# Performance work log

Hardware: AMD Instinct MI355X
Metric: run time of the kernel (lower is better)

Reference implementation:

```python
import jax, jax.numpy as jnp
import numpy as np

B = 4
MAX_N = 2048
D = 512
H = 8
HD = D // H
SRC_LENS = [2048, 1536, 1800, 1200]   # sum = 6584
REF_LENS = [1900, 2048, 1400, 1600]   # sum = 6948
NEG_INF = -1e9


def setup_inputs() -> dict:
    key = jax.random.key(0)
    ks = jax.random.split(key, 8)
    n_src, n_ref = sum(SRC_LENS), sum(REF_LENS)
    s = 0.02
    return {
        "feats_src": jax.random.normal(ks[0], (n_src, D), dtype=jnp.float32),
        "batch_src": jnp.asarray(np.repeat(np.arange(B), SRC_LENS), dtype=jnp.int32),
        "feats_ref": jax.random.normal(ks[1], (n_ref, D), dtype=jnp.float32),
        "batch_ref": jnp.asarray(np.repeat(np.arange(B), REF_LENS), dtype=jnp.int32),
        "w_in": jax.random.normal(ks[2], (3 * D, D), dtype=jnp.float32) * s,
        "b_in": jnp.zeros((3 * D,), dtype=jnp.float32),
        "w_out": jax.random.normal(ks[3], (D, D), dtype=jnp.float32) * s,
        "b_out": jnp.zeros((D,), dtype=jnp.float32),
        "gw1": jax.random.normal(ks[4], (D, D), dtype=jnp.float32) * s,
        "gb1": jnp.zeros((D,), dtype=jnp.float32),
        "gw2": jax.random.normal(ks[5], (1, D), dtype=jnp.float32) * s,
        "gb2": jnp.zeros((1,), dtype=jnp.float32),
    }


def _to_dense(feats, batch_idx):
    # sparse [N, D] (sorted batch indices) -> dense [B, MAX_N, D] + key_padding_mask
    n = feats.shape[0]
    counts = jax.ops.segment_sum(jnp.ones((n,), jnp.int32), batch_idx, num_segments=B)
    starts = jnp.concatenate([jnp.zeros((1,), jnp.int32), jnp.cumsum(counts)[:-1].astype(jnp.int32)])
    pos = jnp.arange(n, dtype=jnp.int32) - starts[batch_idx]  # position within batch
    dense = jnp.zeros((B, MAX_N, feats.shape[1]), feats.dtype).at[batch_idx, pos].set(feats)
    mask = jnp.arange(MAX_N)[None, :] >= counts[:, None]  # True = padding (key_padding_mask)
    return dense, mask, pos


def reference(feats_src, batch_src, feats_ref, batch_ref,
              w_in, b_in, w_out, b_out, gw1, gb1, gw2, gb2):
    d_src, mask_src, pos_src = _to_dense(feats_src, batch_src)
    d_ref, mask_ref, _ = _to_dense(feats_ref, batch_ref)

    # nn.MultiheadAttention (batch_first, eval mode): packed in_proj, scaled dot-product
    q = (d_src @ w_in[:D].T + b_in[:D]).reshape(B, MAX_N, H, HD)
    k = (d_ref @ w_in[D:2 * D].T + b_in[D:2 * D]).reshape(B, MAX_N, H, HD)
    v = (d_ref @ w_in[2 * D:].T + b_in[2 * D:]).reshape(B, MAX_N, H, HD)
    scores = jnp.einsum('bqhd,bkhd->bhqk', q * (HD ** -0.5), k)
    scores = jnp.where(mask_ref[:, None, None, :], NEG_INF, scores)
    attn = jax.nn.softmax(scores, axis=-1)
    ctx = jnp.einsum('bhqk,bkhd->bqhd', attn, v).reshape(B, MAX_N, D)
    d_aligned = ctx @ w_out.T + b_out

    # gate MLP: Linear -> ReLU -> Linear -> Sigmoid
    gate = jax.nn.sigmoid(jax.nn.relu(d_aligned @ gw1.T + gb1) @ gw2.T + gb2)  # [B, MAX_N, 1]
    d_out = d_src + gate * d_aligned

    # dense -> ragged: gather each token back to its flat slot
    out_flat = d_out[batch_src, pos_src]  # [N_src, D]
    return out_flat, gate
```

## Files before the change

### kernel.cpp

```cpp
#include <hip/hip_runtime.h>
#include <hip/hip_bf16.h>


typedef __bf16 bf16x8_t __attribute__((ext_vector_type(8)));
typedef __bf16 bf16x4_t __attribute__((ext_vector_type(4)));
typedef float f32x4_t __attribute__((ext_vector_type(4)));
typedef float f32x2_t __attribute__((ext_vector_type(2)));

#define CQ_SCALE 0.18033688011112042f

__device__ inline bf16x8_t zero8() {
  bf16x8_t z;
#pragma unroll
  for (int t = 0; t < 8; ++t) z[t] = (__bf16)0.0f;
  return z;
}

__device__ __forceinline__ int sniff_f32(const void* w) {
  unsigned short u = ((const unsigned short*)w)[threadIdx.x & 63];
  return __ballot((u & 0x7F80) >= 0x3F80) != 0ULL;
}

__device__ __forceinline__ int2 swz(int bid, int nwg, int nby) {
  int chunk = nwg >> 3;
  int w = (bid & 7) * chunk + (bid >> 3);
  return make_int2(w / nby, w % nby);
}

__global__ void sentinel_k(float* out) {
  if (threadIdx.x == 0 && blockIdx.x == 0) out[0] = 1000.0f;
}

__global__ void cv_all(const void* w_in, const void* b_in, const void* w_out,
                       const void* b_out, const void* gw1, const void* gb1,
                       const void* gw2, const void* gb2,
                       __hip_bfloat16* __restrict__ ws,
                       const void* fs, const void* fr, int do_feats) {
  int f = sniff_f32(w_in);
  int bid = blockIdx.x;
  if (do_feats && bid < 3383) {
    int i = bid * 256 + threadIdx.x;
    const int NFS = 421376;
    const void* src;
    size_t dst;
    int off;
    if (i < NFS) { src = fs; dst = 11803680; off = i * 8; }
    else { src = fr; dst = 15174688; off = (i - NFS) * 8; }
    __hip_bfloat16* d = ws + dst + off;
    if (f) {
      const float* p = (const float*)src + off;
      bf16x8_t v;
#pragma unroll
      for (int e = 0; e < 8; ++e) v[e] = (__bf16)p[e];
      *reinterpret_cast<bf16x8_t*>(d) = v;
    } else {
      *reinterpret_cast<bf16x8_t*>(d) =
          *reinterpret_cast<const bf16x8_t*>((const __hip_bfloat16*)src + off);
    }
    return;
  }
  int base = do_feats ? 3383 : 0;
  int nb = gridDim.x - base;
  const size_t F_W_IN = 16, F_B_IN = 786448, F_W_OUT = 787984, F_B_OUT = 1050128,
               F_GW1 = 1050640, F_GB1 = 1312784, F_GW2 = 1313296, F_GB2 = 1313808;
  const int total = 1313793;
  for (int g = (bid - base) * 256 + threadIdx.x; g < total; g += nb * 256) {
    const void* src;
    size_t dst;
    int i;
    if (g < 786432) { src = w_in; dst = F_W_IN; i = g; }
    else if (g < 787968) { src = b_in; dst = F_B_IN; i = g - 786432; }
    else if (g < 1050112) { src = w_out; dst = F_W_OUT; i = g - 787968; }
    else if (g < 1050624) { src = b_out; dst = F_B_OUT; i = g - 1050112; }
    else if (g < 1312768) { src = gw1; dst = F_GW1; i = g - 1050624; }
    else if (g < 1313280) { src = gb1; dst = F_GB1; i = g - 1312768; }
    else if (g < 1313792) { src = gw2; dst = F_GW2; i = g - 1313280; }
    else { src = gb2; dst = F_GB2; i = g - 1313792; }
    ws[dst + i] = f ? __float2bfloat16(((const float*)src)[i])
                    : ((const __hip_bfloat16*)src)[i];
  }
}

__device__ __forceinline__ void gemm_core(
    const void* __restrict__ A_, long aoff, const __hip_bfloat16* __restrict__ Bt,
    const __hip_bfloat16* __restrict__ bias, __hip_bfloat16* __restrict__ C,
    int M, int K, int lda, int ldc, float cscale, int relu, int f, int bm, int bn,
    long chs, __bf16 (&As)[128][72], __bf16 (&Bs)[128][72]) {
  int tid = threadIdx.x, lane = tid & 63, wave = tid >> 6;
  int wm = wave >> 1, wn = wave & 1;
  int l15 = lane & 15, quad = lane >> 4;

  f32x4_t acc[4][4];
#pragma unroll
  for (int i = 0; i < 4; ++i)
#pragma unroll
    for (int j = 0; j < 4; ++j)
#pragma unroll
      for (int r = 0; r < 4; ++r) acc[i][j][r] = 0.f;

  bf16x8_t ra[4], rb[4];
  f32x4_t raf[4][2];

  auto gload = [&](int k0) {
#pragma unroll
    for (int s = 0; s < 4; ++s) {
      int id = s * 256 + tid;
      int row = id >> 3, col = (id & 7) * 8;
      int arow = bm + row;
      if (f) {
        if (arow < M) {
          const float* p = (const float*)A_ + aoff + (size_t)arow * lda + k0 + col;
          raf[s][0] = *reinterpret_cast<const f32x4_t*>(p);
          raf[s][1] = *reinterpret_cast<const f32x4_t*>(p + 4);
        } else {
#pragma unroll
          for (int e = 0; e < 4; ++e) { raf[s][0][e] = 0.f; raf[s][1][e] = 0.f; }
        }
      } else {
        ra[s] = (arow < M)
                    ? *reinterpret_cast<const bf16x8_t*>((const __hip_bfloat16*)A_ + aoff +
                                                         (size_t)arow * lda + k0 + col)
                    : zero8();
      }
      rb[s] = *reinterpret_cast<const bf16x8_t*>(Bt + (size_t)(bn + row) * 512 + k0 + col);
    }
  };
  auto stage = [&]() {
#pragma unroll
    for (int s = 0; s < 4; ++s) {
      int id = s * 256 + tid;
      int row = id >> 3, col = (id & 7) * 8;
      if (f) {
        bf16x8_t t;
#pragma unroll
        for (int e = 0; e < 4; ++e) {
          t[e] = (__bf16)raf[s][0][e];
          t[4 + e] = (__bf16)raf[s][1][e];
        }
        *reinterpret_cast<bf16x8_t*>(&As[row][col]) = t;
      } else {
        *reinterpret_cast<bf16x8_t*>(&As[row][col]) = ra[s];
      }
      *reinterpret_cast<bf16x8_t*>(&Bs[row][col]) = rb[s];
    }
  };

  int nk = K >> 6;
  gload(0);
  for (int it = 0; it < nk; ++it) {
    stage();
    __syncthreads();
    if (it + 1 < nk) gload((it + 1) * 64);
#pragma unroll
    for (int ks = 0; ks < 2; ++ks) {
      bf16x8_t af[4], bfv[4];
#pragma unroll
      for (int i = 0; i < 4; ++i)
        af[i] = *reinterpret_cast<const bf16x8_t*>(
            &As[wm * 64 + i * 16 + l15][ks * 32 + quad * 8]);
#pragma unroll
      for (int j = 0; j < 4; ++j)
        bfv[j] = *reinterpret_cast<const bf16x8_t*>(
            &Bs[wn * 64 + j * 16 + l15][ks * 32 + quad * 8]);
#pragma unroll
      for (int i = 0; i < 4; ++i)
#pragma unroll
        for (int j = 0; j < 4; ++j)
          acc[i][j] = __builtin_amdgcn_mfma_f32_16x16x32_bf16(af[i], bfv[j], acc[i][j], 0, 0, 0);
    }
    __syncthreads();
  }

#pragma unroll
  for (int i = 0; i < 4; ++i)
#pragma unroll
    for (int j = 0; j < 4; ++j) {
      int col = bn + wn * 64 + j * 16 + l15;
      float bv = __bfloat162float(bias[col]);
#pragma unroll
      for (int r = 0; r < 4; ++r) {
        int row = bm + wm * 64 + i * 16 + quad * 4 + r;
        if (row < M) {
          float v = (acc[i][j][r] + bv) * cscale;
          if (relu) v = fmaxf(v, 0.f);
          size_t idx = chs ? ((size_t)(col >> 6) * chs + (size_t)row * 64 + (col & 63))
                           : ((size_t)row * ldc + col);
          C[idx] = __float2bfloat16(v);
        }
      }
    }
}

__global__ __launch_bounds__(256) void proj2(
    const void* __restrict__ fs, const void* __restrict__ fr,
    const __hip_bfloat16* __restrict__ ws, __hip_bfloat16* __restrict__ Q,
    __hip_bfloat16* __restrict__ KV, const void* snf) {
  __shared__ __bf16 As[128][72];
  __shared__ __bf16 Bs[128][72];
  const size_t F_W_IN = 16, F_B_IN = 786448;
  const long CHS = (long)6948 * 64;
  int f = snf ? sniff_f32(snf) : 0;
  int bid = blockIdx.x;
  if (bid < 208) {
    int2 s = swz(bid, 208, 4);
    gemm_core(fs, 0, ws + F_W_IN, ws + F_B_IN, Q, 6584, 512, 512, 512, CQ_SCALE, 0, f,
              s.x * 128, s.y * 128, 0, As, Bs);
  } else {
    int2 s = swz(bid - 208, 440, 8);
    gemm_core(fr, 0, ws + F_W_IN + 262144, ws + F_B_IN + 512, KV, 6948, 512, 512, 1024,
              1.0f, 0, f, s.x * 128, s.y * 128, CHS, As, Bs);
  }
}

__global__ __launch_bounds__(256) void gemm128z(
    const __hip_bfloat16* __restrict__ A, const __hip_bfloat16* __restrict__ Bt,
    const __hip_bfloat16* __restrict__ bias, __hip_bfloat16* __restrict__ C,
    int M, float cscale, int relu) {
  __shared__ __bf16 As[128][72];
  __shared__ __bf16 Bs[128][72];
  int2 s = swz(blockIdx.x, gridDim.x, 4);
  gemm_core(A, 0, Bt, bias, C, M, 512, 512, 512, cscale, relu, 0,
            s.x * 128, s.y * 128, 0, As, Bs);
}

template <bool AF32>
__global__ __launch_bounds__(256) void gemm128(
    const void* __restrict__ A_, long aoff, const __hip_bfloat16* __restrict__ Bt,
    const __hip_bfloat16* __restrict__ bias, __hip_bfloat16* __restrict__ C,
    int M, int K, int lda, int ldc, float cscale, int relu, long chs,
    const void* snf) {
  __shared__ __bf16 As[128][72];
  __shared__ __bf16 Bs[128][72];
  int f = 0;
  if constexpr (AF32) f = sniff_f32(snf);
  gemm_core(A_, aoff, Bt, bias, C, M, K, lda, ldc, cscale, relu, f,
            blockIdx.x * 128, blockIdx.y * 128, chs, As, Bs);
}

__global__ __launch_bounds__(256) void gate_gemm(
    const __hip_bfloat16* __restrict__ A, const __hip_bfloat16* __restrict__ Bt,
    const __hip_bfloat16* __restrict__ bias, const __hip_bfloat16* __restrict__ gw2,
    float* __restrict__ z4, int M) {
  __shared__ __bf16 As[128][72];
  __shared__ __bf16 Bs[128][72];
  __shared__ float zsc[128][2];
  int tid = threadIdx.x, lane = tid & 63, wave = tid >> 6;
  int wm = wave >> 1, wn = wave & 1;
  int l15 = lane & 15, quad = lane >> 4;
  int2 sw = swz(blockIdx.x, 208, 4);
  int bm = sw.x * 128, bn = sw.y * 128;

  f32x4_t acc[4][4];
#pragma unroll
  for (int i = 0; i < 4; ++i)
#pragma unroll
    for (int j = 0; j < 4; ++j)
#pragma unroll
      for (int r = 0; r < 4; ++r) acc[i][j][r] = 0.f;

  bf16x8_t ra[4], rb[4];
  auto gload = [&](int k0) {
#pragma unroll
    for (int s = 0; s < 4; ++s) {
      int id = s * 256 + tid;
      int row = id >> 3, col = (id & 7) * 8;
      int arow = bm + row;
      ra[s] = (arow < M)
                  ? *reinterpret_cast<const bf16x8_t*>(A + (size_t)arow * 512 + k0 + col)
                  : zero8();
      rb[s] = *reinterpret_cast<const bf16x8_t*>(Bt + (size_t)(bn + row) * 512 + k0 + col);
    }
  };
  auto stage = [&]() {
#pragma unroll
    for (int s = 0; s < 4; ++s) {
      int id = s * 256 + tid;
      int row = id >> 3, col = (id & 7) * 8;
      *reinterpret_cast<bf16x8_t*>(&As[row][col]) = ra[s];
      *reinterpret_cast<bf16x8_t*>(&Bs[row][col]) = rb[s];
    }
  };

  gload(0);
  for (int it = 0; it < 8; ++it) {
    stage();
    __syncthreads();
    if (it + 1 < 8) gload((it + 1) * 64);
#pragma unroll
    for (int ks = 0; ks < 2; ++ks) {
      bf16x8_t af[4], bfv[4];
#pragma unroll
      for (int i = 0; i < 4; ++i)
        af[i] = *reinterpret_cast<const bf16x8_t*>(
            &As[wm * 64 + i * 16 + l15][ks * 32 + quad * 8]);
#pragma unroll
      for (int j = 0; j < 4; ++j)
        bfv[j] = *reinterpret_cast<const bf16x8_t*>(
            &Bs[wn * 64 + j * 16 + l15][ks * 32 + quad * 8]);
#pragma unroll
      for (int i = 0; i < 4; ++i)
#pragma unroll
        for (int j = 0; j < 4; ++j)
          acc[i][j] = __builtin_amdgcn_mfma_f32_16x16x32_bf16(af[i], bfv[j], acc[i][j], 0, 0, 0);
    }
    __syncthreads();
  }

  float zp[4][4];
#pragma unroll
  for (int i = 0; i < 4; ++i)
#pragma unroll
    for (int r = 0; r < 4; ++r) zp[i][r] = 0.f;
#pragma unroll
  for (int i = 0; i < 4; ++i)
#pragma unroll
    for (int j = 0; j < 4; ++j) {
      int col = bn + wn * 64 + j * 16 + l15;
      float bv = __bfloat162float(bias[col]);
      float w2 = __bfloat162float(gw2[col]);
#pragma unroll
      for (int r = 0; r < 4; ++r) {
        float v = fmaxf(acc[i][j][r] + bv, 0.f);
        zp[i][r] += v * w2;
      }
    }
#pragma unroll
  for (int i = 0; i < 4; ++i)
#pragma unroll
    for (int r = 0; r < 4; ++r) {
#pragma unroll
      for (int o = 1; o <= 8; o <<= 1) zp[i][r] += __shfl_xor(zp[i][r], o);
    }
  if (l15 == 0) {
#pragma unroll
    for (int i = 0; i < 4; ++i)
#pragma unroll
      for (int r = 0; r < 4; ++r)
        zsc[wm * 64 + i * 16 + quad * 4 + r][wn] = zp[i][r];
  }
  __syncthreads();
  if (tid < 128) {
    int row = bm + tid;
    if (row < M) z4[sw.y * 6592 + row] = zsc[tid][0] + zsc[tid][1];
  }
}

template <int NS>
__global__ __launch_bounds__(256) void gemm128_pv(
    const __hip_bfloat16* __restrict__ P, const float* __restrict__ L,
    const __hip_bfloat16* __restrict__ Bt, const __hip_bfloat16* __restrict__ bias,
    __hip_bfloat16* __restrict__ C, int M) {
  const size_t PSZ = 3375104;
  __shared__ __bf16 As[128][72];
  __shared__ __bf16 Bs[128][72];
  int tid = threadIdx.x, lane = tid & 63, wave = tid >> 6;
  int wm = wave >> 1, wn = wave & 1;
  int l15 = lane & 15, quad = lane >> 4;
  int2 sw = swz(blockIdx.x, 208, 4);
  int bm = sw.x * 128, bn = sw.y * 128;

  f32x4_t acc[4][4];
#pragma unroll
  for (int i = 0; i < 4; ++i)
#pragma unroll
    for (int j = 0; j < 4; ++j)
#pragma unroll
      for (int r = 0; r < 4; ++r) acc[i][j][r] = 0.f;

  bf16x8_t rp[NS][4], rb[4];
  float rl[4][NS];

  auto gload = [&](int k0) {
    int h = k0 >> 6;
#pragma unroll
    for (int s = 0; s < 4; ++s) {
      int id = s * 256 + tid;
      int row = id >> 3, col = (id & 7) * 8;
      int arow = bm + row;
      if (arow < M) {
        size_t off = (size_t)arow * 512 + k0 + col;
#pragma unroll
        for (int i = 0; i < NS; ++i)
          rp[i][s] = *reinterpret_cast<const bf16x8_t*>(P + i * PSZ + off);
        const float* lp = &L[((size_t)arow * 8 + h) * NS];
#pragma unroll
        for (int i = 0; i < NS; ++i) rl[s][i] = lp[i];
      } else {
#pragma unroll
        for (int i = 0; i < NS; ++i) rp[i][s] = zero8();
        rl[s][0] = 1.f;
#pragma unroll
        for (int i = 1; i < NS; ++i) rl[s][i] = 0.f;
      }
      rb[s] = *reinterpret_cast<const bf16x8_t*>(Bt + (size_t)(bn + row) * 512 + k0 + col);
    }
  };
  auto stage = [&]() {
#pragma unroll
    for (int s = 0; s < 4; ++s) {
      int id = s * 256 + tid;
      int row = id >> 3, col = (id & 7) * 8;
      float sum = 0.f;
#pragma unroll
      for (int i = 0; i < NS; ++i) sum += rl[s][i];
      float sc = 1.0f / sum;
      bf16x8_t t;
#pragma unroll
      for (int e = 0; e < 8; ++e) {
        float v = 0.f;
#pragma unroll
        for (int i = 0; i < NS; ++i) v += rl[s][i] * (float)rp[i][s][e];
        t[e] = (__bf16)(v * sc);
      }
      *reinterpret_cast<bf16x8_t*>(&As[row][col]) = t;
      *reinterpret_cast<bf16x8_t*>(&Bs[row][col]) = rb[s];
    }
  };

  gload(0);
  for (int it = 0; it < 8; ++it) {
    stage();
    __syncthreads();
    if (it + 1 < 8) gload((it + 1) * 64);
#pragma unroll
    for (int ks = 0; ks < 2; ++ks) {
      bf16x8_t af[4], bfv[4];
#pragma unroll
      for (int i = 0; i < 4; ++i)
        af[i] = *reinterpret_cast<const bf16x8_t*>(
            &As[wm * 64 + i * 16 + l15][ks * 32 + quad * 8]);
#pragma unroll
      for (int j = 0; j < 4; ++j)
        bfv[j] = *reinterpret_cast<const bf16x8_t*>(
            &Bs[wn * 64 + j * 16 + l15][ks * 32 + quad * 8]);
#pragma unroll
      for (int i = 0; i < 4; ++i)
#pragma unroll
        for (int j = 0; j < 4; ++j)
          acc[i][j] = __builtin_amdgcn_mfma_f32_16x16x32_bf16(af[i], bfv[j], acc[i][j], 0, 0, 0);
    }
    __syncthreads();
  }

#pragma unroll
  for (int i = 0; i < 4; ++i)
#pragma unroll
    for (int j = 0; j < 4; ++j) {
      int col = bn + wn * 64 + j * 16 + l15;
      float bv = __bfloat162float(bias[col]);
#pragma unroll
      for (int r = 0; r < 4; ++r) {
        int row = bm + wm * 64 + i * 16 + quad * 4 + r;
        if (row < M)
          C[(size_t)row * 512 + col] = __float2bfloat16(acc[i][j][r] + bv);
      }
    }
}

__device__ __forceinline__ void flash_core(
    const __hip_bfloat16* __restrict__ Qb, const __hip_bfloat16* __restrict__ Kb,
    const __hip_bfloat16* __restrict__ Vb, __hip_bfloat16* __restrict__ OUTb,
    float* __restrict__ LPb, int lns, int nsrc, int nref, int qt, int kt0,
    int ktNfull, int do_tail, __bf16 (&KsL)[2][64][68], __bf16 (&VtL)[2][64][72],
    __bf16 (&PL)[4][32][68]) {
  int h = blockIdx.y;
  int tid = threadIdx.x, lane = tid & 63, wave = tid >> 6;
  int l15 = lane & 15, quad = lane >> 4;
  int Mb = nsrc + 1;
  int qbase = qt * 128 + wave * 32;

  bf16x8_t qfr[2][2];
#pragma unroll
  for (int g = 0; g < 2; ++g) {
    int qrow = qbase + g * 16 + l15;
#pragma unroll
    for (int ks = 0; ks < 2; ++ks)
      qfr[g][ks] = (qrow < nsrc)
                       ? *reinterpret_cast<const bf16x8_t*>(
                             Qb + (size_t)qrow * 512 + h * 64 + ks * 32 + quad * 8)
                       : zero8();
  }

  f32x4_t O[2][4];
#pragma unroll
  for (int g = 0; g < 2; ++g)
#pragma unroll
    for (int j = 0; j < 4; ++j)
#pragma unroll
      for (int r = 0; r < 4; ++r) O[g][j][r] = 0.f;

  f32x4_t Lacc[2];
#pragma unroll
  for (int g = 0; g < 2; ++g)
#pragma unroll
    for (int r = 0; r < 4; ++r) Lacc[g][r] = 0.f;
  bf16x8_t ones;
#pragma unroll
  for (int t = 0; t < 8; ++t) ones[t] = (__bf16)1.0f;

  auto load64pair = [&](const __bf16* p) {
    bf16x4_t lo = *reinterpret_cast<const bf16x4_t*>(p);
    bf16x4_t hi = *reinterpret_cast<const bf16x4_t*>(p + 4);
    bf16x8_t v;
#pragma unroll
    for (int e = 0; e < 4; ++e) {
      v[e] = lo[e];
      v[4 + e] = hi[e];
    }
    return v;
  };

  bf16x8_t krA[2], v0, v1;
  auto gloadK = [&](int k0) {
    const __hip_bfloat16* base = Kb + (size_t)k0 * 64 + tid * 16;
    krA[0] = *reinterpret_cast<const bf16x8_t*>(base);
    krA[1] = *reinterpret_cast<const bf16x8_t*>(base + 8);
  };
  auto stageK = [&](int buf) {
#pragma unroll
    for (int p = 0; p < 2; ++p) {
      int lin = tid * 16 + p * 8;
      int row = lin >> 6, col = lin & 63;
      *reinterpret_cast<bf16x4_t*>(&KsL[buf][row][col]) =
          *reinterpret_cast<const bf16x4_t*>(&krA[p]);
      bf16x4_t hi;
#pragma unroll
      for (int e = 0; e < 4; ++e) hi[e] = krA[p][4 + e];
      *reinterpret_cast<bf16x4_t*>(&KsL[buf][row][col + 4]) = hi;
    }
  };
  auto loadV = [&](int k0) {
    const __hip_bfloat16* vp = Vb + (size_t)(k0 + lane) * 64 + wave * 16;
    v0 = *reinterpret_cast<const bf16x8_t*>(vp);
    v1 = *reinterpret_cast<const bf16x8_t*>(vp + 8);
  };

  int nit = ktNfull - kt0;
  if (nit > 0) {
    gloadK(kt0 * 64);
    loadV(kt0 * 64);
  }

  int buf = 0;
  for (int it = 0; it < nit; ++it) {
    int k0 = (kt0 + it) * 64;
    stageK(buf);
    {
      __bf16(*Vt)[72] = VtL[buf];
#pragma unroll
      for (int e = 0; e < 8; ++e) {
        Vt[wave * 16 + e][lane] = v0[e];
        Vt[wave * 16 + 8 + e][lane] = v1[e];
      }
    }
    __syncthreads();
    if (it + 1 < nit) {
      gloadK(k0 + 64);
      loadV(k0 + 64);
    }

    bf16x8_t kf[8];
#pragma unroll
    for (int j = 0; j < 4; ++j)
#pragma unroll
      for (int ks = 0; ks < 2; ++ks)
        kf[j * 2 + ks] = load64pair(&KsL[buf][j * 16 + l15][ks * 32 + quad * 8]);
#pragma unroll
    for (int g = 0; g < 2; ++g) {
      f32x4_t St[4];
#pragma unroll
      for (int j = 0; j < 4; ++j)
#pragma unroll
        for (int r = 0; r < 4; ++r) St[j][r] = 0.f;
#pragma unroll
      for (int j = 0; j < 4; ++j)
#pragma unroll
        for (int ks = 0; ks < 2; ++ks)
          St[j] = __builtin_amdgcn_mfma_f32_16x16x32_bf16(kf[j * 2 + ks], qfr[g][ks],
                                                          St[j], 0, 0, 0);
#pragma unroll
      for (int j = 0; j < 4; ++j) {
        bf16x4_t pk;
#pragma unroll
        for (int r = 0; r < 4; ++r) pk[r] = (__bf16)exp2f(St[j][r]);
        *reinterpret_cast<bf16x4_t*>(&PL[wave][g * 16 + l15][j * 16 + quad * 4]) = pk;
      }
    }

    bf16x8_t pa[2][2];
#pragma unroll
    for (int g = 0; g < 2; ++g)
#pragma unroll
      for (int ks = 0; ks < 2; ++ks)
        pa[g][ks] = load64pair(&PL[wave][g * 16 + l15][ks * 32 + quad * 8]);
#pragma unroll
    for (int g = 0; g < 2; ++g)
#pragma unroll
      for (int ks = 0; ks < 2; ++ks)
        Lacc[g] = __builtin_amdgcn_mfma_f32_16x16x32_bf16(pa[g][ks], ones, Lacc[g], 0, 0, 0);
#pragma unroll
    for (int j = 0; j < 4; ++j)
#pragma unroll
      for (int ks = 0; ks < 2; ++ks) {
        bf16x8_t vbf = *reinterpret_cast<const bf16x8_t*>(
            &VtL[buf][j * 16 + l15][ks * 32 + quad * 8]);
#pragma unroll
        for (int g = 0; g < 2; ++g)
          O[g][j] = __builtin_amdgcn_mfma_f32_16x16x32_bf16(pa[g][ks], vbf, O[g][j], 0, 0, 0);
      }
    __syncthreads();
    buf ^= 1;
  }

  if (do_tail) {
    int k0 = ktNfull * 64;
    __bf16(*Vt)[72] = VtL[buf];
    {
      int kr = k0 + lane;
      const __hip_bfloat16* vp = Vb + (size_t)kr * 64 + wave * 16;
      bf16x8_t t0 = (kr < nref) ? *reinterpret_cast<const bf16x8_t*>(vp) : zero8();
      bf16x8_t t1 = (kr < nref) ? *reinterpret_cast<const bf16x8_t*>(vp + 8) : zero8();
#pragma unroll
      for (int e = 0; e < 8; ++e) {
        Vt[wave * 16 + e][lane] = t0[e];
        Vt[wave * 16 + 8 + e][lane] = t1[e];
      }
    }
    bf16x8_t kf[8];
#pragma unroll
    for (int j = 0; j < 4; ++j) {
      int kcol = k0 + j * 16 + l15;
      const __hip_bfloat16* kp = Kb + (size_t)kcol * 64 + quad * 8;
      kf[j * 2] = (kcol < nref) ? *reinterpret_cast<const bf16x8_t*>(kp) : zero8();
      kf[j * 2 + 1] = (kcol < nref) ? *reinterpret_cast<const bf16x8_t*>(kp + 32) : zero8();
    }
#pragma unroll
    for (int g = 0; g < 2; ++g) {
      f32x4_t St[4];
#pragma unroll
      for (int j = 0; j < 4; ++j)
#pragma unroll
        for (int r = 0; r < 4; ++r) St[j][r] = 0.f;
#pragma unroll
      for (int j = 0; j < 4; ++j)
#pragma unroll
        for (int ks = 0; ks < 2; ++ks)
          St[j] = __builtin_amdgcn_mfma_f32_16x16x32_bf16(kf[j * 2 + ks], qfr[g][ks],
                                                          St[j], 0, 0, 0);
#pragma unroll
      for (int j = 0; j < 4; ++j) {
        bf16x4_t pk;
#pragma unroll
        for (int r = 0; r < 4; ++r) {
          int kl = k0 + j * 16 + quad * 4 + r;
          pk[r] = (__bf16)((kl < nref) ? exp2f(St[j][r]) : 0.f);
        }
        *reinterpret_cast<bf16x4_t*>(&PL[wave][g * 16 + l15][j * 16 + quad * 4]) = pk;
      }
    }
    __syncthreads();
    bf16x8_t pa[2][2];
#pragma unroll
    for (int g = 0; g < 2; ++g)
#pragma unroll
      for (int ks = 0; ks < 2; ++ks)
        pa[g][ks] = load64pair(&PL[wave][g * 16 + l15][ks * 32 + quad * 8]);
#pragma unroll
    for (int g = 0; g < 2; ++g)
#pragma unroll
      for (int ks = 0; ks < 2; ++ks)
        Lacc[g] = __builtin_amdgcn_mfma_f32_16x16x32_bf16(pa[g][ks], ones, Lacc[g], 0, 0, 0);
#pragma unroll
    for (int j = 0; j < 4; ++j)
#pragma unroll
      for (int ks = 0; ks < 2; ++ks) {
        bf16x8_t vbf =
            *reinterpret_cast<const bf16x8_t*>(&Vt[j * 16 + l15][ks * 32 + quad * 8]);
#pragma unroll
        for (int g = 0; g < 2; ++g)
          O[g][j] = __builtin_amdgcn_mfma_f32_16x16x32_bf16(pa[g][ks], vbf, O[g][j], 0, 0, 0);
      }
  }

  if (LPb && l15 == 0) {
#pragma unroll
    for (int g = 0; g < 2; ++g)
#pragma unroll
      for (int r = 0; r < 4; ++r) {
        int row = qbase + g * 16 + quad * 4 + r;
        if (row < Mb) LPb[((size_t)row * 8 + h) * lns] = Lacc[g][r];
      }
  }

#pragma unroll
  for (int g = 0; g < 2; ++g)
#pragma unroll
    for (int r = 0; r < 4; ++r) {
      int row = qbase + g * 16 + quad * 4 + r;
      if (row < Mb) {
        float inv = 1.0f / Lacc[g][r];
#pragma unroll
        for (int j = 0; j < 4; ++j)
          OUTb[(size_t)row * 512 + h * 64 + j * 16 + l15] =
              __float2bfloat16(O[g][j][r] * inv);
      }
    }
}

__global__ __launch_bounds__(256, 3) void flash_all(
    const __hip_bfloat16* __restrict__ Q, const __hip_bfloat16* __restrict__ KV,
    __hip_bfloat16* __restrict__ P, float* __restrict__ L, int zbase, int nsplit) {
  const int TILE_START[4] = {0, 17, 30, 45};
  const int SRC_START[4] = {0, 2048, 3584, 5384};
  const int REF_START[4] = {0, 1900, 3948, 5348};
  const int SRC_LEN[4] = {2048, 1536, 1800, 1200};
  const int REF_LEN[4] = {1900, 2048, 1400, 1600};
  const int CS[4] = {0, 2049, 3586, 5387};
  const size_t PSZ = 3375104;
  const size_t CHS = (size_t)6948 * 64;
  __shared__ __bf16 KsL[2][64][68];
  __shared__ __bf16 VtL[2][64][72];
  __shared__ __bf16 PL[4][32][68];
  int bid = blockIdx.x;
  int b = (bid >= TILE_START[3]) ? 3 : (bid >= TILE_START[2]) ? 2 : (bid >= TILE_START[1]) ? 1 : 0;
  int qt = bid - TILE_START[b];
  int nref = REF_LEN[b];
  int full = nref >> 6, nkt = (nref + 63) >> 6, rem = nref & 63;
  int split = zbase;
  int kt0 = (nkt * split) / nsplit;
  int ktN, tail;
  if (split == nsplit - 1) { ktN = full; tail = rem > 0; }
  else { ktN = (nkt * (split + 1)) / nsplit; tail = 0; }
  int h = blockIdx.y;
  const __hip_bfloat16* Kb = KV + (size_t)h * CHS + (size_t)REF_START[b] * 64;
  const __hip_bfloat16* Vb = KV + (size_t)(8 + h) * CHS + (size_t)REF_START[b] * 64;
  __hip_bfloat16* OUT = P + (size_t)split * PSZ;
  float* LP = (nsplit == 1) ? nullptr : (L + split + (size_t)CS[b] * 8 * nsplit);
  flash_core(Q + (size_t)SRC_START[b] * 512, Kb, Vb, OUT + (size_t)CS[b] * 512, LP,
             nsplit, SRC_LEN[b], nref, qt, kt0, ktN, tail, KsL, VtL, PL);
}

__global__ __launch_bounds__(256, 3) void flash_one(const __hip_bfloat16* __restrict__ Qb,
                                                    const __hip_bfloat16* __restrict__ KVb,
                                                    __hip_bfloat16* __restrict__ OUTb,
                                                    int nsrc, int nref, long chs) {
  __shared__ __bf16 KsL[2][64][68];
  __shared__ __bf16 VtL[2][64][72];
  __shared__ __bf16 PL[4][32][68];
  int h = blockIdx.y;
  const __hip_bfloat16* Kb = KVb + (size_t)h * chs;
  const __hip_bfloat16* Vb = KVb + (size_t)(8 + h) * chs;
  flash_core(Qb, Kb, Vb, OUTb, nullptr, 1, nsrc, nref, blockIdx.x, 0, nref >> 6,
             (nref & 63) > 0, KsL, VtL, PL);
}

__global__ __launch_bounds__(256) void finalize_all(
    const void* __restrict__ src, const __hip_bfloat16* __restrict__ aligned,
    const float* __restrict__ z4, const __hip_bfloat16* __restrict__ gb2,
    void* __restrict__ out, const void* snf) {
  int f = sniff_f32(snf);
  int lane = threadIdx.x & 63;
  int r = blockIdx.x * 4 + (threadIdx.x >> 6);
  int b = (r >= 5387) ? 3 : (r >= 3586) ? 2 : (r >= 2049) ? 1 : 0;
  const int CS[4] = {0, 2049, 3586, 5387};
  const int NSRC[4] = {2048, 1536, 1800, 1200};
  int pos = r - CS[b];
  int c0 = lane * 8;

  float z = z4[r] + z4[6592 + r] + z4[2 * 6592 + r] + z4[3 * 6592 + r] +
            __bfloat162float(gb2[0]);
  float g = 1.f / (1.f + __expf(-z));

  const size_t GOFF = (size_t)6584 * 512;
  if (pos < NSRC[b]) {
    size_t ib = (size_t)(r - b) * 512 + c0;
    bf16x8_t av = *reinterpret_cast<const bf16x8_t*>(aligned + (size_t)r * 512 + c0);
    if (f) {
      const float* sp = (const float*)src + ib;
      f32x4_t s0 = *reinterpret_cast<const f32x4_t*>(sp);
      f32x4_t s1 = *reinterpret_cast<const f32x4_t*>(sp + 4);
      f32x4_t o0, o1;
#pragma unroll
      for (int e = 0; e < 4; ++e) {
        o0[e] = s0[e] + g * __bfloat162float(av[e]);
        o1[e] = s1[e] + g * __bfloat162float(av[4 + e]);
      }
      float* op = (float*)out + ib;
      *reinterpret_cast<f32x4_t*>(op) = o0;
      *reinterpret_cast<f32x4_t*>(op + 4) = o1;
    } else {
      bf16x8_t sv = *reinterpret_cast<const bf16x8_t*>((const __hip_bfloat16*)src + ib);
      bf16x8_t ov;
#pragma unroll
      for (int e = 0; e < 8; ++e)
        ov[e] = (__bf16)(__bfloat162float(sv[e]) + g * __bfloat162float(av[e]));
      *reinterpret_cast<bf16x8_t*>((__hip_bfloat16*)out + ib) = ov;
    }
    if (lane == 0) {
      size_t go = GOFF + b * 2048 + pos;
      if (f) ((float*)out)[go] = g;
      else ((__hip_bfloat16*)out)[go] = __float2bfloat16(g);
    }
  } else {
    for (int p = NSRC[b] + lane; p < 2048; p += 64) {
      size_t go = GOFF + b * 2048 + p;
      if (f) ((float*)out)[go] = g;
      else ((__hip_bfloat16*)out)[go] = __float2bfloat16(g);
    }
  }
}

__global__ __launch_bounds__(256) void finalize_b(
    const void* __restrict__ src, const __hip_bfloat16* __restrict__ alnb,
    const __hip_bfloat16* __restrict__ hidb, const __hip_bfloat16* __restrict__ gw2,
    const __hip_bfloat16* __restrict__ gb2, void* __restrict__ out,
    int b, int nsrc, int src_start, const void* snf) {
  int f = sniff_f32(snf);
  int lane = threadIdx.x & 63;
  int r = blockIdx.x * 4 + (threadIdx.x >> 6);
  if (r > nsrc) return;

  float zacc = 0.f;
  const __hip_bfloat16* hrow = hidb + (size_t)r * 512;
#pragma unroll
  for (int t = 0; t < 8; ++t) {
    int c = lane + (t << 6);
    zacc += __bfloat162float(hrow[c]) * __bfloat162float(gw2[c]);
  }
  for (int o = 32; o; o >>= 1) zacc += __shfl_xor(zacc, o);
  zacc += __bfloat162float(gb2[0]);
  float g = 1.f / (1.f + __expf(-zacc));

  const size_t GOFF = (size_t)6584 * 512;
  if (r < nsrc) {
    size_t ib = (size_t)(src_start + r) * 512;
    const __hip_bfloat16* arow = alnb + (size_t)r * 512;
#pragma unroll
    for (int t = 0; t < 8; ++t) {
      int c = lane + (t << 6);
      float sv = f ? ((const float*)src)[ib + c]
                   : __bfloat162float(((const __hip_bfloat16*)src)[ib + c]);
      float val = sv + g * __bfloat162float(arow[c]);
      if (f) ((float*)out)[ib + c] = val;
      else ((__hip_bfloat16*)out)[ib + c] = __float2bfloat16(val);
    }
    if (lane == 0) {
      size_t go = GOFF + b * 2048 + r;
      if (f) ((float*)out)[go] = g;
      else ((__hip_bfloat16*)out)[go] = __float2bfloat16(g);
    }
  } else {
    for (int p = nsrc + lane; p < 2048; p += 64) {
      size_t go = GOFF + b * 2048 + p;
      if (f) ((float*)out)[go] = g;
      else ((__hip_bfloat16*)out)[go] = __float2bfloat16(g);
    }
  }
}

extern "C" void kernel_launch(void* const* d_in, const int* in_sizes, int n_in,
                              void* d_out, int out_size, void* d_ws, size_t ws_size,
                              hipStream_t stream) {
  (void)in_sizes; (void)n_in; (void)out_size;
  const void* feats_src = d_in[0];
  const void* feats_ref = d_in[2];
  const void* w_in = d_in[4];
  const void* b_in = d_in[5];
  const void* w_out = d_in[6];
  const void* b_out = d_in[7];
  const void* gw1 = d_in[8];
  const void* gb1 = d_in[9];
  const void* gw2 = d_in[10];
  const void* gb2 = d_in[11];

  const size_t F_W_IN = 16, F_B_IN = 786448, F_W_OUT = 787984, F_B_OUT = 1050128,
               F_GW1 = 1050640, F_GB1 = 1312784, F_GW2 = 1313296, F_GB2 = 1313808,
               A0 = 1313824;
  const size_t PSZ = 3375104;
  const size_t R3E = A0 + PSZ + 7114752;
  const size_t FS0 = R3E;
  const size_t FR0 = R3E + 3371008;
  const size_t Z4EL = 52736;
  const size_t NEED_A2 = 2 * (R3E + 2 * PSZ + 210816 + Z4EL);
  const size_t NEED_A = 2 * (R3E + PSZ + Z4EL);
  const size_t NEED_B = 2 * (A0 + 4259840);

  if (ws_size < NEED_B) {
    sentinel_k<<<1, 64, 0, stream>>>((float*)d_out);
    return;
  }

  __hip_bfloat16* ws = (__hip_bfloat16*)d_ws;

  const int SRC_LEN[4] = {2048, 1536, 1800, 1200};
  const int REF_LEN[4] = {1900, 2048, 1400, 1600};
  const int SRC_START[4] = {0, 2048, 3584, 5384};
  const int REF_START[4] = {0, 1900, 3948, 5348};
  dim3 blk(256);

  if (ws_size >= NEED_A) {
    __hip_bfloat16* R1 = ws + A0;
    __hip_bfloat16* R2 = R1 + PSZ;
    __hip_bfloat16* R3 = R2 + 7114752;
    int NS = (ws_size >= NEED_A2) ? 2 : 1;
    if (NS == 2) {
      float* L = (float*)(ws + R3E + 2 * PSZ);
      float* Z4 = (float*)(ws + R3E + 2 * PSZ + 210816);
      cv_all<<<dim3(4407), blk, 0, stream>>>(w_in, b_in, w_out, b_out, gw1, gb1,
                                             gw2, gb2, ws, feats_src, feats_ref, 1);
      proj2<<<dim3(648), blk, 0, stream>>>(ws + FS0, ws + FR0, ws, R1, R2, nullptr);
      flash_all<<<dim3(55, 8, 1), blk, 0, stream>>>(R1, R2, R3, L, 0, 2);
      flash_all<<<dim3(55, 8, 1), blk, 0, stream>>>(R1, R2, R3, L, 1, 2);
      gemm128_pv<2><<<dim3(208), blk, 0, stream>>>(R3, L, ws + F_W_OUT,
                                                   ws + F_B_OUT, R1, 6588);
      gate_gemm<<<dim3(208), blk, 0, stream>>>(R1, ws + F_GW1, ws + F_GB1,
                                               ws + F_GW2, Z4, 6588);
      finalize_all<<<dim3(1647), blk, 0, stream>>>(feats_src, R1, Z4, ws + F_GB2,
                                                   d_out, w_in);
    } else {
      float* Z4 = (float*)(ws + R3E + PSZ);
      cv_all<<<dim3(1024), blk, 0, stream>>>(w_in, b_in, w_out, b_out, gw1, gb1,
                                             gw2, gb2, ws, nullptr, nullptr, 0);
      proj2<<<dim3(648), blk, 0, stream>>>(feats_src, feats_ref, ws, R1, R2, w_in);
      flash_all<<<dim3(55, 8, 1), blk, 0, stream>>>(R1, R2, R3, nullptr, 0, 1);
      gemm128z<<<dim3(208), blk, 0, stream>>>(R3, ws + F_W_OUT, ws + F_B_OUT, R1,
                                              6588, 1.0f, 0);
      gate_gemm<<<dim3(208), blk, 0, stream>>>(R1, ws + F_GW1, ws + F_GB1,
                                               ws + F_GW2, Z4, 6588);
      finalize_all<<<dim3(1647), blk, 0, stream>>>(feats_src, R1, Z4, ws + F_GB2,
                                                   d_out, w_in);
    }
  } else {
    cv_all<<<dim3(1024), blk, 0, stream>>>(w_in, b_in, w_out, b_out, gw1, gb1,
                                           gw2, gb2, ws, nullptr, nullptr, 0);
    __hip_bfloat16* W2 = ws + A0;
    __hip_bfloat16* W1 = W2 + 2097152;
    __hip_bfloat16* W3 = W1 + 1081344;
    const long CHS_B = (long)2048 * 64;
    for (int b = 0; b < 4; ++b) {
      int nsrc = SRC_LEN[b], nref = REF_LEN[b];
      gemm128<true><<<dim3((nsrc + 127) / 128, 4), blk, 0, stream>>>(
          feats_src, (long)SRC_START[b] * 512, ws + F_W_IN, ws + F_B_IN, W1, nsrc, 512,
          512, 512, CQ_SCALE, 0, 0, w_in);
      gemm128<true><<<dim3((nref + 127) / 128, 8), blk, 0, stream>>>(
          feats_ref, (long)REF_START[b] * 512, ws + F_W_IN + 262144, ws + F_B_IN + 512,
          W2, nref, 512, 512, 1024, 1.0f, 0, CHS_B, w_in);
      flash_one<<<dim3((nsrc + 128) / 128, 8), blk, 0, stream>>>(W1, W2, W3, nsrc, nref,
                                                                 CHS_B);
      gemm128<false><<<dim3((nsrc + 128) / 128, 4), blk, 0, stream>>>(
          W3, 0, ws + F_W_OUT, ws + F_B_OUT, W1, nsrc + 1, 512, 512, 512, 1.0f, 0, 0,
          nullptr);
      gemm128<false><<<dim3((nsrc + 128) / 128, 4), blk, 0, stream>>>(
          W1, 0, ws + F_GW1, ws + F_GB1, W3, nsrc + 1, 512, 512, 512, 1.0f, 1, 0,
          nullptr);
      finalize_b<<<dim3((nsrc + 4) / 4), blk, 0, stream>>>(
          feats_src, W1, W3, ws + F_GW2, ws + F_GB2, d_out, b, nsrc, SRC_START[b], w_in);
    }
  }
}
```

Measured before the change: 252.9 us.

## Specialize GEMM core for bf16 inputs and merge flash split launches

```diff
diff --git a/kernel.cpp b/kernel.cpp
--- a/kernel.cpp
+++ b/kernel.cpp
@@ -81,6 +81,7 @@
   }
 }
 
+template <bool RTF>
 __device__ __forceinline__ void gemm_core(
     const void* __restrict__ A_, long aoff, const __hip_bfloat16* __restrict__ Bt,
     const __hip_bfloat16* __restrict__ bias, __hip_bfloat16* __restrict__ C,
@@ -99,7 +100,7 @@
       for (int r = 0; r < 4; ++r) acc[i][j][r] = 0.f;
 
   bf16x8_t ra[4], rb[4];
-  f32x4_t raf[4][2];
+  f32x4_t raf[RTF ? 4 : 1][2];
 
   auto gload = [&](int k0) {
 #pragma unroll
@@ -107,19 +108,26 @@
       int id = s * 256 + tid;
       int row = id >> 3, col = (id & 7) * 8;
       int arow = bm + row;
-      if (f) {
-        if (arow < M) {
-          const float* p = (const float*)A_ + aoff + (size_t)arow * lda + k0 + col;
-          raf[s][0] = *reinterpret_cast<const f32x4_t*>(p);
-          raf[s][1] = *reinterpret_cast<const f32x4_t*>(p + 4);
+      if constexpr (RTF) {
+        if (f) {
+          if (arow < M) {
+            const float* p = (const float*)A_ + aoff + (size_t)arow * lda + k0 + col;
+            raf[s][0] = *reinterpret_cast<const f32x4_t*>(p);
+            raf[s][1] = *reinterpret_cast<const f32x4_t*>(p + 4);
+          } else {
+#pragma unroll
+            for (int e = 0; e < 4; ++e) { raf[s][0][e] = 0.f; raf[s][1][e] = 0.f; }
+          }
         } else {
-#pragma unroll
-          for (int e = 0; e < 4; ++e) { raf[s][0][e] = 0.f; raf[s][1][e] = 0.f; }
+          ra[s] = (arow < M)
+                      ? *reinterpret_cast<const bf16x8_t*>(
+                            (const __hip_bfloat16*)A_ + aoff + (size_t)arow * lda + k0 + col)
+                      : zero8();
         }
       } else {
         ra[s] = (arow < M)
-                    ? *reinterpret_cast<const bf16x8_t*>((const __hip_bfloat16*)A_ + aoff +
-                                                         (size_t)arow * lda + k0 + col)
+                    ? *reinterpret_cast<const bf16x8_t*>(
+                          (const __hip_bfloat16*)A_ + aoff + (size_t)arow * lda + k0 + col)
                     : zero8();
       }
       rb[s] = *reinterpret_cast<const bf16x8_t*>(Bt + (size_t)(bn + row) * 512 + k0 + col);
@@ -130,14 +138,18 @@
     for (int s = 0; s < 4; ++s) {
       int id = s * 256 + tid;
       int row = id >> 3, col = (id & 7) * 8;
-      if (f) {
-        bf16x8_t t;
-#pragma unroll
-        for (int e = 0; e < 4; ++e) {
-          t[e] = (__bf16)raf[s][0][e];
-          t[4 + e] = (__bf16)raf[s][1][e];
+      if constexpr (RTF) {
+        if (f) {
+          bf16x8_t t;
+#pragma unroll
+          for (int e = 0; e < 4; ++e) {
+            t[e] = (__bf16)raf[s][0][e];
+            t[4 + e] = (__bf16)raf[s][1][e];
+          }
+          *reinterpret_cast<bf16x8_t*>(&As[row][col]) = t;
+        } else {
+          *reinterpret_cast<bf16x8_t*>(&As[row][col]) = ra[s];
         }
-        *reinterpret_cast<bf16x8_t*>(&As[row][col]) = t;
       } else {
         *reinterpret_cast<bf16x8_t*>(&As[row][col]) = ra[s];
       }
@@ -191,6 +203,26 @@
     }
 }
 
+__global__ __launch_bounds__(256, 3) void proj2b(
+    const __hip_bfloat16* __restrict__ fs, const __hip_bfloat16* __restrict__ fr,
+    const __hip_bfloat16* __restrict__ ws, __hip_bfloat16* __restrict__ Q,
+    __hip_bfloat16* __restrict__ KV) {
+  __shared__ __bf16 As[128][72];
+  __shared__ __bf16 Bs[128][72];
+  const size_t F_W_IN = 16, F_B_IN = 786448;
+  const long CHS = (long)6948 * 64;
+  int bid = blockIdx.x;
+  if (bid < 208) {
+    int2 s = swz(bid, 208, 4);
+    gemm_core<false>(fs, 0, ws + F_W_IN, ws + F_B_IN, Q, 6584, 512, 512, 512, CQ_SCALE,
+                     0, 0, s.x * 128, s.y * 128, 0, As, Bs);
+  } else {
+    int2 s = swz(bid - 208, 440, 8);
+    gemm_core<false>(fr, 0, ws + F_W_IN + 262144, ws + F_B_IN + 512, KV, 6948, 512, 512,
+                     1024, 1.0f, 0, 0, s.x * 128, s.y * 128, CHS, As, Bs);
+  }
+}
+
 __global__ __launch_bounds__(256) void proj2(
     const void* __restrict__ fs, const void* __restrict__ fr,
     const __hip_bfloat16* __restrict__ ws, __hip_bfloat16* __restrict__ Q,
@@ -199,28 +231,28 @@
   __shared__ __bf16 Bs[128][72];
   const size_t F_W_IN = 16, F_B_IN = 786448;
   const long CHS = (long)6948 * 64;
-  int f = snf ? sniff_f32(snf) : 0;
+  int f = sniff_f32(snf);
   int bid = blockIdx.x;
   if (bid < 208) {
     int2 s = swz(bid, 208, 4);
-    gemm_core(fs, 0, ws + F_W_IN, ws + F_B_IN, Q, 6584, 512, 512, 512, CQ_SCALE, 0, f,
-              s.x * 128, s.y * 128, 0, As, Bs);
+    gemm_core<true>(fs, 0, ws + F_W_IN, ws + F_B_IN, Q, 6584, 512, 512, 512, CQ_SCALE,
+                    0, f, s.x * 128, s.y * 128, 0, As, Bs);
   } else {
     int2 s = swz(bid - 208, 440, 8);
-    gemm_core(fr, 0, ws + F_W_IN + 262144, ws + F_B_IN + 512, KV, 6948, 512, 512, 1024,
-              1.0f, 0, f, s.x * 128, s.y * 128, CHS, As, Bs);
-  }
-}
-
-__global__ __launch_bounds__(256) void gemm128z(
+    gemm_core<true>(fr, 0, ws + F_W_IN + 262144, ws + F_B_IN + 512, KV, 6948, 512, 512,
+                    1024, 1.0f, 0, f, s.x * 128, s.y * 128, CHS, As, Bs);
+  }
+}
+
+__global__ __launch_bounds__(256, 3) void gemm128z(
     const __hip_bfloat16* __restrict__ A, const __hip_bfloat16* __restrict__ Bt,
     const __hip_bfloat16* __restrict__ bias, __hip_bfloat16* __restrict__ C,
     int M, float cscale, int relu) {
   __shared__ __bf16 As[128][72];
   __shared__ __bf16 Bs[128][72];
   int2 s = swz(blockIdx.x, gridDim.x, 4);
-  gemm_core(A, 0, Bt, bias, C, M, 512, 512, 512, cscale, relu, 0,
-            s.x * 128, s.y * 128, 0, As, Bs);
+  gemm_core<false>(A, 0, Bt, bias, C, M, 512, 512, 512, cscale, relu, 0,
+                   s.x * 128, s.y * 128, 0, As, Bs);
 }
 
 template <bool AF32>
@@ -233,8 +265,8 @@
   __shared__ __bf16 Bs[128][72];
   int f = 0;
   if constexpr (AF32) f = sniff_f32(snf);
-  gemm_core(A_, aoff, Bt, bias, C, M, K, lda, ldc, cscale, relu, f,
-            blockIdx.x * 128, blockIdx.y * 128, chs, As, Bs);
+  gemm_core<AF32>(A_, aoff, Bt, bias, C, M, K, lda, ldc, cscale, relu, f,
+                  blockIdx.x * 128, blockIdx.y * 128, chs, As, Bs);
 }
 
 __global__ __launch_bounds__(256) void gate_gemm(
@@ -726,7 +758,7 @@
   int qt = bid - TILE_START[b];
   int nref = REF_LEN[b];
   int full = nref >> 6, nkt = (nref + 63) >> 6, rem = nref & 63;
-  int split = zbase;
+  int split = zbase + blockIdx.z;
   int kt0 = (nkt * split) / nsplit;
   int ktN, tail;
   if (split == nsplit - 1) { ktN = full; tail = rem > 0; }
@@ -908,9 +940,8 @@
       float* Z4 = (float*)(ws + R3E + 2 * PSZ + 210816);
       cv_all<<<dim3(4407), blk, 0, stream>>>(w_in, b_in, w_out, b_out, gw1, gb1,
                                              gw2, gb2, ws, feats_src, feats_ref, 1);
-      proj2<<<dim3(648), blk, 0, stream>>>(ws + FS0, ws + FR0, ws, R1, R2, nullptr);
-      flash_all<<<dim3(55, 8, 1), blk, 0, stream>>>(R1, R2, R3, L, 0, 2);
-      flash_all<<<dim3(55, 8, 1), blk, 0, stream>>>(R1, R2, R3, L, 1, 2);
+      proj2b<<<dim3(648), blk, 0, stream>>>(ws + FS0, ws + FR0, ws, R1, R2);
+      flash_all<<<dim3(55, 8, 2), blk, 0, stream>>>(R1, R2, R3, L, 0, 2);
       gemm128_pv<2><<<dim3(208), blk, 0, stream>>>(R3, L, ws + F_W_OUT,
                                                    ws + F_B_OUT, R1, 6588);
       gate_gemm<<<dim3(208), blk, 0, stream>>>(R1, ws + F_GW1, ws + F_GB1,
```

After: 218.4 us. 1.16x faster.
